# Performance work log

Hardware: AMD Instinct MI355X
Metric: run time of the kernel (lower is better)

The kernel has to match this reference:

```python
import jax, jax.numpy as jnp
import numpy as np

N, DIN, D, K0, NC = 32768, 768, 512, 128, 2
KS = [128, 64, 32, 16]  # prototype counts per stage (num_protos // 2**i)
NEG_SLOPE = 0.01


def _lin(x, W, b):
    # torch nn.Linear: W is [out, in]
    return x @ W.T + b


def _ln(x, g, b):
    m = x.mean(-1, keepdims=True)
    v = ((x - m) ** 2).mean(-1, keepdims=True)
    return (x - m) * jax.lax.rsqrt(v + 1e-5) * g + b


def setup_inputs() -> dict:
    key = jax.random.key(0)
    ks = jax.random.split(key, 40)
    s = 0.02

    def nrm(k, shp, sc=s):
        return jax.random.normal(k, shp, jnp.float32) * sc

    inp = {}
    inp["data"] = jax.random.normal(ks[0], (N, DIN), jnp.float32)
    inp["prototypes"] = jax.random.normal(ks[1], (K0, DIN), jnp.float32)
    inp["W_pp"] = nrm(ks[2], (D, DIN)); inp["b_pp"] = jnp.zeros((D,), jnp.float32)
    inp["W_cp"] = nrm(ks[3], (D, DIN)); inp["b_cp"] = jnp.zeros((D,), jnp.float32)
    inp["sim_scale"] = jnp.ones((1,), jnp.float32)
    # 3 enhancer MLPs + layernorms (stacked, same shapes)
    inp["enh_w1"] = nrm(ks[4], (3, D, D)); inp["enh_b1"] = jnp.zeros((3, D), jnp.float32)
    inp["enh_w2"] = nrm(ks[5], (3, D, D)); inp["enh_b2"] = jnp.zeros((3, D), jnp.float32)
    inp["ln_g"] = jnp.ones((3, D), jnp.float32); inp["ln_b"] = jnp.zeros((3, D), jnp.float32)
    # ProtoReducers: Mlp along K axis; fc1 [inK,inK], fc2 [outK,inK]
    ki = 6
    for i in range(3):
        inK, outK = KS[i], KS[i + 1]
        inp[f"red_w1_{i}"] = nrm(ks[ki], (inK, inK)); ki += 1
        inp[f"red_b1_{i}"] = jnp.zeros((inK,), jnp.float32)
        inp[f"red_w2_{i}"] = nrm(ks[ki], (outK, inK)); ki += 1
        inp[f"red_b2_{i}"] = jnp.zeros((outK,), jnp.float32)
    inp["W_proc"] = nrm(ks[20], (D, D)); inp["b_proc"] = jnp.zeros((D,), jnp.float32)
    inp["g_an"] = jnp.ones((D,), jnp.float32); inp["b_an"] = jnp.zeros((D,), jnp.float32)
    inp["W_t"] = nrm(ks[21], (D, D)); inp["b_t"] = jnp.zeros((D,), jnp.float32)
    inp["W_g"] = nrm(ks[22], (D, D)); inp["b_g"] = jnp.zeros((D,), jnp.float32)
    inp["W_s"] = nrm(ks[23], (1, D)); inp["b_s"] = jnp.zeros((1,), jnp.float32)
    inp["W_h"] = nrm(ks[24], (D, D)); inp["b_h"] = jnp.zeros((D,), jnp.float32)
    inp["W_c"] = nrm(ks[25], (NC, D)); inp["b_c"] = jnp.zeros((NC,), jnp.float32)
    return inp


def reference(data, prototypes, W_pp, b_pp, W_cp, b_cp, sim_scale,
              enh_w1, enh_b1, enh_w2, enh_b2, ln_g, ln_b,
              red_w1_0, red_b1_0, red_w2_0, red_b2_0,
              red_w1_1, red_b1_1, red_w2_1, red_b2_1,
              red_w1_2, red_b1_2, red_w2_2, red_b2_2,
              W_proc, b_proc, g_an, b_an,
              W_t, b_t, W_g, b_g, W_s, b_s, W_h, b_h, W_c, b_c):
    # patch / prototype projections (Linear + LeakyReLU)
    P = jax.nn.leaky_relu(_lin(data, W_pp, b_pp), NEG_SLOPE)        # [N, D]
    C = jax.nn.leaky_relu(_lin(prototypes, W_cp, b_cp), NEG_SLOPE)  # [K0, D]
    # denom = max(1e-6, tau * similarity_scale.item()); tau=1, no grad through scale
    denom = jnp.maximum(1e-6, jax.lax.stop_gradient(sim_scale)[0])
    reds = [(red_w1_0, red_b1_0, red_w2_0, red_b2_0),
            (red_w1_1, red_b1_1, red_w2_1, red_b2_1),
            (red_w1_2, red_b1_2, red_w2_2, red_b2_2)]
    for i in range(3):
        # L2 similarity: -cdist(P, C) computed as a GEMM
        d2 = (jnp.sum(P * P, -1, keepdims=True) + jnp.sum(C * C, -1)[None, :]
              - 2.0 * (P @ C.T))
        sim = -jnp.sqrt(jnp.maximum(d2, 1e-12))                     # [N, K]
        A = jax.nn.softmax(sim / denom, axis=1)                     # soft routing
        ctx = A @ C                                                 # [N, D]
        P = _ln(P + ctx, ln_g[i], ln_b[i])
        P = P + _lin(jax.nn.relu(_lin(P, enh_w1[i], enh_b1[i])), enh_w2[i], enh_b2[i])
        # ProtoReducer: Mlp over K axis (operate on C.T of shape [D, K])
        w1, b1, w2, b2 = reds[i]
        Ct = _lin(jax.nn.relu(_lin(C.T, w1, b1)), w2, b2)           # [D, Kout]
        C = Ct.T
    Z = jnp.concatenate([P, C], axis=0)                             # [N+16, D]
    Z = jax.nn.relu(_lin(Z, W_proc, b_proc))
    Z = _ln(Z, g_an, b_an)
    # gated attention MIL pooling
    t = jnp.tanh(_lin(Z, W_t, b_t))
    g = jax.nn.sigmoid(_lin(Z, W_g, b_g))
    scores = _lin(t * g, W_s, b_s)                                  # [N+16, 1]
    Aw = jax.nn.softmax(scores, axis=0)
    bag = Aw.T @ Z                                                  # [1, D]
    h = jax.nn.relu(_lin(bag, W_h, b_h))
    logits = _lin(h, W_c, b_c)                                      # [1, 2]
    return logits
```

## Files before the change

kernel.cpp:

```cpp
#include <hip/hip_runtime.h>
#include <math.h>

typedef _Float16 f16x8 __attribute__((ext_vector_type(8)));
typedef _Float16 f16x4 __attribute__((ext_vector_type(4)));
typedef float f32x4 __attribute__((ext_vector_type(4)));

#define TBM 256
#define TBN 128
#define TBK 32

#define AS1 __attribute__((address_space(1)))
#define AS3 __attribute__((address_space(3)))

__device__ __forceinline__ void gll16(const _Float16* g, _Float16* l)
{
    __builtin_amdgcn_global_load_lds((const AS1 unsigned int*)g,
                                     (AS3 unsigned int*)l, 16, 0, 0);
}

__device__ __forceinline__ int xcd_swz(int d, int nwg)
{
    int q = nwg >> 3, r = nwg & 7;
    int x = d & 7, idx = d >> 3;
    int base = x < r ? x * (q + 1) : r * (q + 1) + (x - r) * q;
    return base + idx;
}

__device__ __forceinline__ float fsigmoid(float x)
{
    return __builtin_amdgcn_rcpf(1.f + __expf(-x));
}
__device__ __forceinline__ float ftanh(float x)
{
    float ax = fabsf(x);
    float e = __expf(-2.f * ax);
    float t = (1.f - e) * __builtin_amdgcn_rcpf(1.f + e);
    return copysignf(t, x);
}

struct CvtSegs {
    const float* src[7];
    _Float16* dst[7];
    int cum4[8];
};

__global__ __launch_bounds__(256)
void cvtall_k(CvtSegs a)
{
    int total = a.cum4[7];
    for (int i = blockIdx.x * 256 + threadIdx.x; i < total; i += gridDim.x * 256) {
        int s = 0;
        while (i >= a.cum4[s + 1]) s++;
        int loc = (i - a.cum4[s]) * 4;
        float4 v = *(const float4*)(a.src[s] + loc);
        f16x4 h = { (_Float16)v.x, (_Float16)v.y, (_Float16)v.z, (_Float16)v.w };
        *(f16x4*)(a.dst[s] + loc) = h;
    }
}

template<int ACT, bool F16OUT>
__global__ __launch_bounds__(256)
void dot_k(const float* __restrict__ X, const float* __restrict__ W,
           const float* __restrict__ bias, void* __restrict__ Yv,
           int M, int K)
{
    int gw = (blockIdx.x * 256 + threadIdx.x) >> 6;
    int lane = threadIdx.x & 63;
    if (gw >= M * 512) return;
    int r = gw >> 9, n = gw & 511;
    const float* xr = X + (size_t)r * K;
    const float* wr = W + (size_t)n * K;
    float d = 0.f;
    for (int t = 0; t < K; t += 256) {
        float4 a = *(const float4*)(xr + t + lane * 4);
        float4 b = *(const float4*)(wr + t + lane * 4);
        d += a.x * b.x + a.y * b.y + a.z * b.z + a.w * b.w;
    }
#pragma unroll
    for (int o = 32; o; o >>= 1) d += __shfl_xor(d, o);
    if (lane == 0) {
        float v = d + bias[n];
        if (ACT == 1) v = v > 0.f ? v : 0.01f * v;
        else if (ACT == 2) v = fmaxf(v, 0.f);
        if (F16OUT) ((_Float16*)Yv)[(size_t)r * 512 + n] = (_Float16)v;
        else        ((float*)Yv)[(size_t)r * 512 + n] = v;
    }
}

__global__ __launch_bounds__(256)
void cvtC2_k(const float* __restrict__ C, _Float16* __restrict__ Ch,
             _Float16* __restrict__ CTh, float* __restrict__ Csq2, int Kin)
{
    int w = threadIdx.x >> 6, lane = threadIdx.x & 63;
    int row = blockIdx.x * 4 + w;
    if (row >= Kin) return;
    float4 a = *(const float4*)(C + (size_t)row * 512 + lane * 8);
    float4 b = *(const float4*)(C + (size_t)row * 512 + lane * 8 + 4);
    f16x8 h;
    h[0] = (_Float16)a.x; h[1] = (_Float16)a.y; h[2] = (_Float16)a.z; h[3] = (_Float16)a.w;
    h[4] = (_Float16)b.x; h[5] = (_Float16)b.y; h[6] = (_Float16)b.z; h[7] = (_Float16)b.w;
    *(f16x8*)(Ch + (size_t)row * 512 + lane * 8) = h;
    float s = 0.f;
#pragma unroll
    for (int q = 0; q < 8; q++) {
        float f = (float)h[q];
        s += f * f;
        CTh[(size_t)(lane * 8 + q) * Kin + row] = h[q];
    }
#pragma unroll
    for (int o = 32; o; o >>= 1) s += __shfl_xor(s, o);
    if (lane == 0) { Csq2[row * 2] = s; Csq2[row * 2 + 1] = 0.f; }
}

template<int MODE, int ACT, bool SQ>
__global__ __launch_bounds__(512)
void mgemm(const _Float16* __restrict__ A, const _Float16* __restrict__ B,
           const float* __restrict__ bias, _Float16* __restrict__ Yh,
           float* __restrict__ Psq4, int M, int K, int Nout)
{
    __shared__ _Float16 As[2][TBM * TBK];
    __shared__ _Float16 Bs[2][TBN * TBK];
    const int tid = threadIdx.x;
    const int lane = tid & 63;
    const int wid = tid >> 6;
    const int wr = wid >> 1, wc = wid & 1;

    int bid = xcd_swz(blockIdx.y * gridDim.x + blockIdx.x, gridDim.x * gridDim.y);
    const int m0 = (bid / gridDim.x) * TBM;
    const int n0 = (bid % gridDim.x) * TBN;

    f32x4 acc[4][4] = {};
    const int nt = K / TBK;

    const int lrow = lane >> 2;
    const int lk = (lane & 3) * 8;

    auto stage = [&](int t, int buf) {
        const int k0 = t * TBK;
#pragma unroll
        for (int q = 0; q < 2; q++) {
            int c = wid * 2 + q;
            int r = c * 16 + lrow;
            int am = min(m0 + r, M - 1);
            gll16(A + (size_t)am * K + k0 + lk, &As[buf][c * 512]);
        }
        {
            int c = wid;
            int r = c * 16 + lrow;
            int bn = min(n0 + r, Nout - 1);
            gll16(B + (size_t)bn * K + k0 + lk, &Bs[buf][c * 512]);
        }
    };

    stage(0, 0);
    __syncthreads();
    for (int t = 0; t < nt; ++t) {
        const int cur = t & 1;
        if (t + 1 < nt) stage(t + 1, cur ^ 1);
        f16x8 af[4], bf[4];
#pragma unroll
        for (int mi = 0; mi < 4; mi++)
            af[mi] = *(const f16x8*)(&As[cur][(wr * 64 + mi * 16 + (lane & 15)) * TBK + (lane >> 4) * 8]);
#pragma unroll
        for (int nj = 0; nj < 4; nj++)
            bf[nj] = *(const f16x8*)(&Bs[cur][(wc * 64 + nj * 16 + (lane & 15)) * TBK + (lane >> 4) * 8]);
#pragma unroll
        for (int mi = 0; mi < 4; mi++)
#pragma unroll
            for (int nj = 0; nj < 4; nj++)
                acc[mi][nj] = __builtin_amdgcn_mfma_f32_16x16x32_f16(af[mi], bf[nj], acc[mi][nj], 0, 0, 0);
        __syncthreads();
    }

    _Float16* eb = &As[0][0];
    const int g = lane >> 4;
#pragma unroll
    for (int p = 0; p < 2; p++) {
        if (p) __syncthreads();
        if ((wr >> 1) == p) {
#pragma unroll
            for (int nj = 0; nj < 4; nj++) {
                int col = wc * 64 + nj * 16 + (lane & 15);
                float bv = bias ? bias[n0 + col] : 0.f;
#pragma unroll
                for (int mi = 0; mi < 4; mi++)
#pragma unroll
                    for (int r = 0; r < 4; r++) {
                        int lr = (wr & 1) * 64 + mi * 16 + g * 4 + r;
                        float v = acc[mi][nj][r] + bv;
                        if (MODE == 0) {
                            if (ACT == 1) v = v > 0.f ? v : 0.01f * v;
                            else if (ACT == 2) v = fmaxf(v, 0.f);
                        }
                        eb[lr * 128 + col] = (_Float16)v;
                    }
            }
        }
        __syncthreads();
        int t4 = tid * 4;
        int lr = t4 >> 4;
        int cbase = (t4 & 15) * 8;
        int m = m0 + p * 128 + lr;
        float sq = 0.f;
        if (m < M) {
#pragma unroll
            for (int q = 0; q < 4; q++) {
                int c0 = cbase + q * 8;
                f16x8 hv = *(f16x8*)(eb + lr * 128 + c0);
                size_t gidx = (size_t)m * Nout + n0 + c0;
                if (MODE == 1) {
                    f16x8 old = *(f16x8*)(Yh + gidx);
                    f16x8 nw;
#pragma unroll
                    for (int e = 0; e < 8; e++) {
                        float s = (float)old[e] + (float)hv[e];
                        nw[e] = (_Float16)s;
                    }
                    *(f16x8*)(Yh + gidx) = nw;
                    hv = nw;
                } else {
                    *(f16x8*)(Yh + gidx) = hv;
                }
                if (SQ) {
#pragma unroll
                    for (int e = 0; e < 8; e++) { float f = (float)hv[e]; sq += f * f; }
                }
            }
        }
        if (SQ) {
            sq += __shfl_xor(sq, 1);
            sq += __shfl_xor(sq, 2);
            if ((lane & 3) == 0 && m < M) Psq4[(size_t)m * 4 + (n0 >> 7)] = sq;
        }
    }
}

__global__ __launch_bounds__(512)
void ctxln_k(const _Float16* __restrict__ A, const _Float16* __restrict__ CT,
             const float* __restrict__ g, const float* __restrict__ b,
             _Float16* __restrict__ Ph, int M, int Kin)
{
    __shared__ _Float16 As[2][128 * TBK];
    __shared__ _Float16 Bs[2][512 * TBK];
    const int tid = threadIdx.x;
    const int lane = tid & 63;
    const int wid = tid >> 6;
    const int wr = wid >> 2, wc = wid & 3;
    const int m0 = blockIdx.y * 128;

    f32x4 acc[4][8] = {};
    const int nt = Kin / TBK;

    const int lrow = lane >> 2;
    const int lk = (lane & 3) * 8;

    auto stage = [&](int t, int buf) {
        const int k0 = t * TBK;
        {
            int r = wid * 16 + lrow;
            gll16(A + (size_t)(m0 + r) * Kin + k0 + lk, &As[buf][wid * 512]);
        }
#pragma unroll
        for (int q = 0; q < 4; q++) {
            int c = wid * 4 + q;
            int n = c * 16 + lrow;
            gll16(CT + (size_t)n * Kin + k0 + lk, &Bs[buf][c * 512]);
        }
    };

    stage(0, 0);
    __syncthreads();
    for (int t = 0; t < nt; ++t) {
        const int cur = t & 1;
        if (t + 1 < nt) stage(t + 1, cur ^ 1);
        f16x8 af[4], bf[8];
#pragma unroll
        for (int mi = 0; mi < 4; mi++)
            af[mi] = *(const f16x8*)(&As[cur][(wr * 64 + mi * 16 + (lane & 15)) * TBK + (lane >> 4) * 8]);
#pragma unroll
        for (int nj = 0; nj < 8; nj++)
            bf[nj] = *(const f16x8*)(&Bs[cur][(wc * 128 + nj * 16 + (lane & 15)) * TBK + (lane >> 4) * 8]);
#pragma unroll
        for (int mi = 0; mi < 4; mi++)
#pragma unroll
            for (int nj = 0; nj < 8; nj++)
                acc[mi][nj] = __builtin_amdgcn_mfma_f32_16x16x32_f16(af[mi], bf[nj], acc[mi][nj], 0, 0, 0);
        __syncthreads();
    }

    _Float16* eb = &Bs[0][0];
    const int gq = lane >> 4;
#pragma unroll
    for (int p = 0; p < 2; p++) {
        if (p) __syncthreads();
        if (wr == p) {
#pragma unroll
            for (int nj = 0; nj < 8; nj++) {
                int col = wc * 128 + nj * 16 + (lane & 15);
#pragma unroll
                for (int mi = 0; mi < 4; mi++)
#pragma unroll
                    for (int r = 0; r < 4; r++) {
                        int lr = mi * 16 + gq * 4 + r;
                        eb[lr * 512 + col] = (_Float16)acc[mi][nj][r];
                    }
            }
        }
        __syncthreads();
#pragma unroll
        for (int rr = 0; rr < 8; rr++) {
            int lr = wid * 8 + rr;
            int m = m0 + p * 64 + lr;
            f16x8 cv = *(f16x8*)(eb + lr * 512 + lane * 8);
            f16x8 pv = *(const f16x8*)(Ph + (size_t)m * 512 + lane * 8);
            float v[8];
            float s = 0.f, ss = 0.f;
#pragma unroll
            for (int q = 0; q < 8; q++) {
                v[q] = (float)pv[q] + (float)cv[q];
                s += v[q]; ss += v[q] * v[q];
            }
#pragma unroll
            for (int o = 32; o; o >>= 1) { s += __shfl_xor(s, o); ss += __shfl_xor(ss, o); }
            float mean = s * (1.f / 512.f);
            float var = ss * (1.f / 512.f) - mean * mean;
            float inv = 1.f / sqrtf(var + 1e-5f);
            int d0 = lane * 8;
            f16x8 o8;
#pragma unroll
            for (int q = 0; q < 8; q++)
                o8[q] = (_Float16)((v[q] - mean) * inv * g[d0 + q] + b[d0 + q]);
            *(f16x8*)(Ph + (size_t)m * 512 + d0) = o8;
        }
    }
}

__global__ __launch_bounds__(512)
void procln_k(const _Float16* __restrict__ A, const _Float16* __restrict__ W,
              const float* __restrict__ bias, const float* __restrict__ g,
              const float* __restrict__ b, _Float16* __restrict__ Zh, int M)
{
    __shared__ _Float16 As[2][128 * TBK];
    __shared__ _Float16 Bs[2][512 * TBK];
    const int tid = threadIdx.x;
    const int lane = tid & 63;
    const int wid = tid >> 6;
    const int wr = wid >> 2, wc = wid & 3;
    const int m0 = blockIdx.y * 128;
    const int K = 512;

    f32x4 acc[4][8] = {};
    const int nt = K / TBK;

    const int lrow = lane >> 2;
    const int lk = (lane & 3) * 8;

    auto stage = [&](int t, int buf) {
        const int k0 = t * TBK;
        {
            int r = wid * 16 + lrow;
            gll16(A + (size_t)(m0 + r) * K + k0 + lk, &As[buf][wid * 512]);
        }
#pragma unroll
        for (int q = 0; q < 4; q++) {
            int c = wid * 4 + q;
            int n = c * 16 + lrow;
            gll16(W + (size_t)n * K + k0 + lk, &Bs[buf][c * 512]);
        }
    };

    stage(0, 0);
    __syncthreads();
    for (int t = 0; t < nt; ++t) {
        const int cur = t & 1;
        if (t + 1 < nt) stage(t + 1, cur ^ 1);
        f16x8 af[4], bf[8];
#pragma unroll
        for (int mi = 0; mi < 4; mi++)
            af[mi] = *(const f16x8*)(&As[cur][(wr * 64 + mi * 16 + (lane & 15)) * TBK + (lane >> 4) * 8]);
#pragma unroll
        for (int nj = 0; nj < 8; nj++)
            bf[nj] = *(const f16x8*)(&Bs[cur][(wc * 128 + nj * 16 + (lane & 15)) * TBK + (lane >> 4) * 8]);
#pragma unroll
        for (int mi = 0; mi < 4; mi++)
#pragma unroll
            for (int nj = 0; nj < 8; nj++)
                acc[mi][nj] = __builtin_amdgcn_mfma_f32_16x16x32_f16(af[mi], bf[nj], acc[mi][nj], 0, 0, 0);
        __syncthreads();
    }

    _Float16* eb = &Bs[0][0];
    const int gq = lane >> 4;
#pragma unroll
    for (int p = 0; p < 2; p++) {
        if (p) __syncthreads();
        if (wr == p) {
#pragma unroll
            for (int nj = 0; nj < 8; nj++) {
                int col = wc * 128 + nj * 16 + (lane & 15);
                float bv = bias[col];
#pragma unroll
                for (int mi = 0; mi < 4; mi++)
#pragma unroll
                    for (int r = 0; r < 4; r++) {
                        int lr = mi * 16 + gq * 4 + r;
                        eb[lr * 512 + col] = (_Float16)fmaxf(acc[mi][nj][r] + bv, 0.f);
                    }
            }
        }
        __syncthreads();
#pragma unroll
        for (int rr = 0; rr < 8; rr++) {
            int lr = wid * 8 + rr;
            int m = m0 + p * 64 + lr;
            f16x8 cv = *(f16x8*)(eb + lr * 512 + lane * 8);
            float v[8];
            float s = 0.f, ss = 0.f;
#pragma unroll
            for (int q = 0; q < 8; q++) {
                v[q] = (float)cv[q];
                s += v[q]; ss += v[q] * v[q];
            }
#pragma unroll
            for (int o = 32; o; o >>= 1) { s += __shfl_xor(s, o); ss += __shfl_xor(ss, o); }
            float mean = s * (1.f / 512.f);
            float var = ss * (1.f / 512.f) - mean * mean;
            float inv = 1.f / sqrtf(var + 1e-5f);
            int d0 = lane * 8;
            f16x8 o8;
#pragma unroll
            for (int q = 0; q < 8; q++)
                o8[q] = (_Float16)((v[q] - mean) * inv * g[d0 + q] + b[d0 + q]);
            *(f16x8*)(Zh + (size_t)m * 512 + d0) = o8;
        }
    }
}

__global__ __launch_bounds__(512)
void gatgemm(const _Float16* __restrict__ A, const _Float16* __restrict__ B1,
             const _Float16* __restrict__ B2, const float* __restrict__ c1,
             const float* __restrict__ c2, const float* __restrict__ Ws,
             float* __restrict__ scr4, int M, int K, int Nout)
{
    __shared__ _Float16 As[2][TBM * TBK];
    __shared__ _Float16 B1s[2][TBN * TBK];
    __shared__ _Float16 B2s[2][TBN * TBK];
    const int tid = threadIdx.x;
    const int lane = tid & 63;
    const int wid = tid >> 6;
    const int wr = wid >> 1, wc = wid & 1;

    int bid = xcd_swz(blockIdx.y * gridDim.x + blockIdx.x, gridDim.x * gridDim.y);
    const int m0 = (bid / gridDim.x) * TBM;
    const int n0 = (bid % gridDim.x) * TBN;

    f32x4 acc1[4][4] = {};
    f32x4 acc2[4][4] = {};
    const int nt = K / TBK;

    const int lrow = lane >> 2;
    const int lk = (lane & 3) * 8;

    auto stage = [&](int t, int buf) {
        const int k0 = t * TBK;
#pragma unroll
        for (int q = 0; q < 2; q++) {
            int c = wid * 2 + q;
            int r = c * 16 + lrow;
            int am = min(m0 + r, M - 1);
            gll16(A + (size_t)am * K + k0 + lk, &As[buf][c * 512]);
        }
        {
            int c = wid;
            int r = c * 16 + lrow;
            int bn = min(n0 + r, Nout - 1);
            gll16(B1 + (size_t)bn * K + k0 + lk, &B1s[buf][c * 512]);
            gll16(B2 + (size_t)bn * K + k0 + lk, &B2s[buf][c * 512]);
        }
    };

    stage(0, 0);
    __syncthreads();
    for (int t = 0; t < nt; ++t) {
        const int cur = t & 1;
        if (t + 1 < nt) stage(t + 1, cur ^ 1);
        f16x8 af[4], bf1[4], bf2[4];
#pragma unroll
        for (int mi = 0; mi < 4; mi++)
            af[mi] = *(const f16x8*)(&As[cur][(wr * 64 + mi * 16 + (lane & 15)) * TBK + (lane >> 4) * 8]);
#pragma unroll
        for (int nj = 0; nj < 4; nj++) {
            int ro = (wc * 64 + nj * 16 + (lane & 15)) * TBK + (lane >> 4) * 8;
            bf1[nj] = *(const f16x8*)(&B1s[cur][ro]);
            bf2[nj] = *(const f16x8*)(&B2s[cur][ro]);
        }
#pragma unroll
        for (int mi = 0; mi < 4; mi++)
#pragma unroll
            for (int nj = 0; nj < 4; nj++) {
                acc1[mi][nj] = __builtin_amdgcn_mfma_f32_16x16x32_f16(af[mi], bf1[nj], acc1[mi][nj], 0, 0, 0);
                acc2[mi][nj] = __builtin_amdgcn_mfma_f32_16x16x32_f16(af[mi], bf2[nj], acc2[mi][nj], 0, 0, 0);
            }
        __syncthreads();
    }

    const int g = lane >> 4;
    float wsv[4];
#pragma unroll
    for (int nj = 0; nj < 4; nj++)
        wsv[nj] = Ws[n0 + wc * 64 + nj * 16 + (lane & 15)];
#pragma unroll
    for (int mi = 0; mi < 4; mi++) {
#pragma unroll
        for (int r = 0; r < 4; r++) {
            float p = 0.f;
#pragma unroll
            for (int nj = 0; nj < 4; nj++) {
                int col = n0 + wc * 64 + nj * 16 + (lane & 15);
                float t1 = ftanh(acc1[mi][nj][r] + c1[col]);
                float g1 = fsigmoid(acc2[mi][nj][r] + c2[col]);
                p += t1 * g1 * wsv[nj];
            }
#pragma unroll
            for (int o = 1; o < 16; o <<= 1) p += __shfl_xor(p, o);
            if ((lane & 15) == 0) {
                int m = m0 + wr * 64 + mi * 16 + g * 4 + r;
                if (m < M) scr4[(size_t)m * 4 + (n0 >> 7)] = p;
            }
        }
    }
}

#define SBM 128
__global__ __launch_bounds__(256)
void simgemm(const _Float16* __restrict__ A, const _Float16* __restrict__ B,
             const float* __restrict__ Psq4, const float* __restrict__ Csq2,
             const float* __restrict__ sscale, _Float16* __restrict__ Ah,
             int M, int K)
{
    const int Kin = 128;
    __shared__ _Float16 As[2][SBM * TBK];
    __shared__ _Float16 Bs[2][SBM * TBK];
    __shared__ float redmx[2][SBM];
    __shared__ float redsm[2][SBM];
    const int tid = threadIdx.x;
    const int lane = tid & 63;
    const int wid = tid >> 6;
    const int wr = wid >> 1, wc = wid & 1;
    const int m0 = blockIdx.y * SBM;

    f32x4 acc[4][4] = {};
    const int nt = K / TBK;
    const int lrow = lane >> 2;
    const int lk = (lane & 3) * 8;

    auto stage = [&](int t, int buf) {
        const int k0 = t * TBK;
#pragma unroll
        for (int q = 0; q < 2; q++) {
            int c = wid * 2 + q;
            int r = c * 16 + lrow;
            gll16(A + (size_t)(m0 + r) * K + k0 + lk, &As[buf][c * 512]);
            gll16(B + (size_t)r * K + k0 + lk, &Bs[buf][c * 512]);
        }
    };

    stage(0, 0);
    __syncthreads();
    for (int t = 0; t < nt; ++t) {
        const int cur = t & 1;
        if (t + 1 < nt) stage(t + 1, cur ^ 1);
        f16x8 af[4], bf[4];
#pragma unroll
        for (int mi = 0; mi < 4; mi++)
            af[mi] = *(const f16x8*)(&As[cur][(wr * 64 + mi * 16 + (lane & 15)) * TBK + (lane >> 4) * 8]);
#pragma unroll
        for (int nj = 0; nj < 4; nj++)
            bf[nj] = *(const f16x8*)(&Bs[cur][(wc * 64 + nj * 16 + (lane & 15)) * TBK + (lane >> 4) * 8]);
#pragma unroll
        for (int mi = 0; mi < 4; mi++)
#pragma unroll
            for (int nj = 0; nj < 4; nj++)
                acc[mi][nj] = __builtin_amdgcn_mfma_f32_16x16x32_f16(af[mi], bf[nj], acc[mi][nj], 0, 0, 0);
        __syncthreads();
    }

// ... 225 lines not shown
}

__global__ __launch_bounds__(1024)
void pool_k(const float4* __restrict__ s4, float* __restrict__ s,
            float* __restrict__ scal, int M)
{
    __shared__ float sm[16];
    int tid = threadIdx.x, lane = tid & 63, wid = tid >> 6;
    float mx = -INFINITY;
    for (int i = tid; i < M; i += 1024) {
        float4 a = s4[i];
        float v = (a.x + a.y) + (a.z + a.w);
        s[i] = v;
        mx = fmaxf(mx, v);
    }
#pragma unroll
    for (int o = 32; o; o >>= 1) mx = fmaxf(mx, __shfl_xor(mx, o));
    if (lane == 0) sm[wid] = mx;
    __syncthreads();
    if (wid == 0) {
        float v = (lane < 16) ? sm[lane] : -INFINITY;
#pragma unroll
        for (int o = 8; o; o >>= 1) v = fmaxf(v, __shfl_xor(v, o));
        if (lane == 0) sm[0] = v;
    }
    __syncthreads();
    float gmax = sm[0];
    __syncthreads();
    float sum = 0.f;
    for (int i = tid; i < M; i += 1024) {
        float e = __expf(s[i] - gmax);
        s[i] = e;
        sum += e;
    }
#pragma unroll
    for (int o = 32; o; o >>= 1) sum += __shfl_xor(sum, o);
    if (lane == 0) sm[wid] = sum;
    __syncthreads();
    if (tid == 0) {
        float t = 0.f;
        for (int w = 0; w < 16; w++) t += sm[w];
        scal[0] = t;
    }
}

__global__ __launch_bounds__(256)
void bagp_k(const _Float16* __restrict__ Z, const float* __restrict__ w,
            float* __restrict__ PB, int M, int cs)
{
    int d = blockIdx.x * 256 + threadIdx.x;
    int chunk = blockIdx.y;
    int i0 = chunk * cs;
    int i1 = min(M, i0 + cs);
    float acc = 0.f;
    for (int i = i0; i < i1; i++) acc = fmaf(w[i], (float)Z[(size_t)i * 512 + d], acc);
    PB[(size_t)chunk * 512 + d] = acc;
}

__global__ __launch_bounds__(256)
void bagf_k(const float* __restrict__ PB, const float* __restrict__ scal,
            float* __restrict__ bag, int nchunk)
{
    int d = blockIdx.x * 256 + threadIdx.x;
    float acc = 0.f;
    for (int c = 0; c < nchunk; c++) acc += PB[(size_t)c * 512 + d];
    bag[d] = acc / scal[0];
}

__global__ __launch_bounds__(256)
void h_k(const float* __restrict__ bag, const float* __restrict__ Wh,
         const float* __restrict__ bh, float* __restrict__ h)
{
    int wid = threadIdx.x >> 6, lane = threadIdx.x & 63;
    int j = blockIdx.x * 4 + wid;
    const float* wr = Wh + (size_t)j * 512;
    float d = 0.f;
#pragma unroll
    for (int t = 0; t < 2; t++) {
        float4 a = *(const float4*)(wr + t * 256 + lane * 4);
        float4 bv = *(const float4*)(bag + t * 256 + lane * 4);
        d += a.x * bv.x + a.y * bv.y + a.z * bv.z + a.w * bv.w;
    }
#pragma unroll
    for (int o = 32; o; o >>= 1) d += __shfl_xor(d, o);
    if (lane == 0) h[j] = fmaxf(d + bh[j], 0.f);
}

__global__ __launch_bounds__(128)
void logit_k(const float* __restrict__ h, const float* __restrict__ Wc,
             const float* __restrict__ bc, float* __restrict__ out)
{
    int wid = threadIdx.x >> 6, lane = threadIdx.x & 63;
    const float* wr = Wc + (size_t)wid * 512;
    float d = 0.f;
#pragma unroll
    for (int t = 0; t < 2; t++) {
        float4 a = *(const float4*)(wr + t * 256 + lane * 4);
        float4 hv = *(const float4*)(h + t * 256 + lane * 4);
        d += a.x * hv.x + a.y * hv.y + a.z * hv.z + a.w * hv.w;
    }
#pragma unroll
    for (int o = 32; o; o >>= 1) d += __shfl_xor(d, o);
    if (lane == 0) out[wid] = d + bc[wid];
}

extern "C" void kernel_launch(void* const* d_in, const int* in_sizes, int n_in,
                              void* d_out, int out_size, void* d_ws, size_t ws_size,
                              hipStream_t stream)
{
    const float* data    = (const float*)d_in[0];
    const float* protos  = (const float*)d_in[1];
    const float* W_pp    = (const float*)d_in[2];
    const float* b_pp    = (const float*)d_in[3];
    const float* W_cp    = (const float*)d_in[4];
    const float* b_cp    = (const float*)d_in[5];
    const float* sscale  = (const float*)d_in[6];
    const float* enh_w1  = (const float*)d_in[7];
    const float* enh_b1  = (const float*)d_in[8];
    const float* enh_w2  = (const float*)d_in[9];
    const float* enh_b2  = (const float*)d_in[10];
    const float* ln_g    = (const float*)d_in[11];
    const float* ln_b    = (const float*)d_in[12];
    const float* red_w1[3] = {(const float*)d_in[13], (const float*)d_in[17], (const float*)d_in[21]};
    const float* red_b1[3] = {(const float*)d_in[14], (const float*)d_in[18], (const float*)d_in[22]};
    const float* red_w2[3] = {(const float*)d_in[15], (const float*)d_in[19], (const float*)d_in[23]};
    const float* red_b2[3] = {(const float*)d_in[16], (const float*)d_in[20], (const float*)d_in[24]};
    const float* W_proc  = (const float*)d_in[25];
    const float* b_proc  = (const float*)d_in[26];
    const float* g_an    = (const float*)d_in[27];
    const float* b_an    = (const float*)d_in[28];
    const float* W_t     = (const float*)d_in[29];
    const float* b_t     = (const float*)d_in[30];
    const float* W_g     = (const float*)d_in[31];
    const float* b_g     = (const float*)d_in[32];
    const float* W_s     = (const float*)d_in[33];
    const float* b_s     = (const float*)d_in[34];
    const float* W_h     = (const float*)d_in[35];
    const float* b_h     = (const float*)d_in[36];
    const float* W_c     = (const float*)d_in[37];
    const float* b_c     = (const float*)d_in[38];
    float* out = (float*)d_out;
    (void)b_s;

    constexpr int N = 32768, DIN = 768, D = 512;
    constexpr int NCHUNK = 256;
    char* w = (char*)d_ws;
    auto alloc = [&](size_t bytes) -> char* {
        char* p = w; w += (bytes + 255) & ~(size_t)255; return p;
    };
    _Float16* Ph     = (_Float16*)alloc((size_t)N * D * 2);
    _Float16* TMPh   = (_Float16*)alloc((size_t)N * D * 2);
    _Float16* Zh     = (_Float16*)alloc((size_t)(N + 16) * D * 2);
    _Float16* Ztail  = (_Float16*)alloc((size_t)16 * D * 2);
    _Float16* datah  = (_Float16*)alloc((size_t)N * DIN * 2);
    _Float16* Ah     = (_Float16*)alloc((size_t)N * 128 * 2);
    _Float16* Ch     = (_Float16*)alloc(128 * D * 2);
    _Float16* CTh    = (_Float16*)alloc(128 * D * 2);
    _Float16* Wpph   = (_Float16*)alloc((size_t)D * DIN * 2);
    _Float16* w1h    = (_Float16*)alloc((size_t)3 * D * D * 2);
    _Float16* w2h    = (_Float16*)alloc((size_t)3 * D * D * 2);
    _Float16* Wproch = (_Float16*)alloc((size_t)D * D * 2);
    _Float16* Wth    = (_Float16*)alloc((size_t)D * D * 2);
    _Float16* Wgh    = (_Float16*)alloc((size_t)D * D * 2);
    float*    Psq4   = (float*)alloc((size_t)N * 4 * 4);
    float*    Csq2   = (float*)alloc(128 * 2 * 4);
    float*    Ca     = (float*)alloc(128 * D * 4);
    float*    Cb     = (float*)alloc(128 * D * 4);
    float*    H1     = (float*)alloc(128 * D * 4);
    float*    scr4   = (float*)alloc((size_t)(N + 16) * 4 * 4);
    float*    scr    = (float*)alloc((size_t)(N + 16) * 4);
    float*    PB     = (float*)alloc((size_t)NCHUNK * D * 4);
    float*    bag    = (float*)alloc(D * 4);
    float*    hb     = (float*)alloc(D * 4);
    float*    scal   = (float*)alloc(8 * 4);

    dim3 blk(256);
    dim3 blk512(512);
    auto mgrid = [](int M_, int Nout_) { return dim3((Nout_ + TBN - 1) / TBN, (M_ + TBM - 1) / TBM); };

    {
        CvtSegs cs;
        const float* srcs[7] = { data, W_pp, enh_w1, enh_w2, W_proc, W_t, W_g };
        _Float16* dsts[7]    = { datah, Wpph, w1h, w2h, Wproch, Wth, Wgh };
        int sizes[7] = { N * DIN, D * DIN, 3 * D * D, 3 * D * D, D * D, D * D, D * D };
        int c = 0;
        cs.cum4[0] = 0;
        for (int s = 0; s < 7; s++) {
            cs.src[s] = srcs[s]; cs.dst[s] = dsts[s];
            c += sizes[s] / 4;
            cs.cum4[s + 1] = c;
        }
        cvtall_k<<<dim3(4096), blk, 0, stream>>>(cs);
    }

    mgemm<0, 1, true><<<mgrid(N, D), blk512, 0, stream>>>(datah, Wpph, b_pp, Ph, Psq4, N, DIN, D);
    dot_k<1, false><<<dim3(128 * 512 / 4), blk, 0, stream>>>(protos, W_cp, b_cp, Ca, 128, DIN);
    cvtC2_k<<<dim3(32), blk, 0, stream>>>(Ca, Ch, CTh, Csq2, 128);

    float* C = Ca;
    float* Cn = Cb;
    int Kin = 128;
    for (int i = 0; i < 3; i++) {
        int Kout = Kin >> 1;
        if (i == 0)
            simgemm<<<dim3(1, N / SBM), blk, 0, stream>>>(Ph, Ch, Psq4, Csq2, sscale, Ah, N, D);
        else if (i == 1)
            simgemm_s<64><<<dim3(1, N / 256), blk, 0, stream>>>(Ph, Ch, Psq4, Csq2, sscale, Ah, N, D);
        else
            simgemm_s<32><<<dim3(1, N / 256), blk, 0, stream>>>(Ph, Ch, Psq4, Csq2, sscale, Ah, N, D);
        ctxln_k<<<dim3(1, N / 128), blk512, 0, stream>>>(Ah, CTh, ln_g + (size_t)i * D, ln_b + (size_t)i * D, Ph, N, Kin);
        mgemm<0, 2, false><<<mgrid(N, D), blk512, 0, stream>>>(Ph, w1h + (size_t)i * D * D, enh_b1 + (size_t)i * D, TMPh, nullptr, N, D, D);
        if (i < 2)
            mgemm<1, 0, true><<<mgrid(N, D), blk512, 0, stream>>>(TMPh, w2h + (size_t)i * D * D, enh_b2 + (size_t)i * D, Ph, Psq4, N, D, D);
        else
            mgemm<1, 0, false><<<mgrid(N, D), blk512, 0, stream>>>(TMPh, w2h + (size_t)i * D * D, enh_b2 + (size_t)i * D, Ph, nullptr, N, D, D);
        red1_k<<<dim3(2, Kin), blk, 0, stream>>>(C, red_w1[i], red_b1[i], H1, Kin);
        red2_k<<<dim3(2, Kout), blk, 0, stream>>>(H1, red_w2[i], red_b2[i], Cn, Ch, CTh, Csq2, Kin, Kout);
        float* t = C; C = Cn; Cn = t;
        Kin = Kout;
    }

    procln_k<<<dim3(1, N / 128), blk512, 0, stream>>>(Ph, Wproch, b_proc, g_an, b_an, Zh, N);
    dot_k<2, true><<<dim3(16 * 512 / 4), blk, 0, stream>>>(C, W_proc, b_proc, Ztail, 16, D);
    ln_k<<<dim3(4), blk, 0, stream>>>(Ztail, nullptr, g_an, b_an, Zh + (size_t)N * D, 16);

    gatgemm<<<mgrid(N + 16, D), blk512, 0, stream>>>(Zh, Wth, Wgh, b_t, b_g, W_s, scr4, N + 16, D, D);

    pool_k<<<dim3(1), dim3(1024), 0, stream>>>((const float4*)scr4, scr, scal, N + 16);
    int cs2 = (N + 16 + NCHUNK - 1) / NCHUNK;
    bagp_k<<<dim3(2, NCHUNK), blk, 0, stream>>>(Zh, scr, PB, N + 16, cs2);
    bagf_k<<<dim3(2), blk, 0, stream>>>(PB, scal, bag, NCHUNK);

    h_k<<<dim3(128), blk, 0, stream>>>(bag, W_h, b_h, hb);
    logit_k<<<dim3(1), dim3(128), 0, stream>>>(hb, W_c, b_c, out);
}
```

Before: 772.5 us.

## Fuse fp32-to-fp16 conversion of input data into the first projection GEMM

The separate pass that converted the 32768x768 fp32 data matrix to fp16 is removed, and a new GEMM kernel reads fp32 data directly, converts in registers and writes fp16 into LDS. This drops one full write and re-read of the fp16 copy of the data. In exchange the A-tile loads become synchronous register loads instead of direct global-to-LDS loads, which reduces overlap inside the GEMM and doubles the bytes read for A. The conversion kernel's grid is also halved since it now only handles weights.

```diff
diff --git a/kernel.cpp b/kernel.cpp
--- a/kernel.cpp
+++ b/kernel.cpp
@@ -39,15 +39,15 @@
 }
 
 struct CvtSegs {
-    const float* src[7];
-    _Float16* dst[7];
-    int cum4[8];
+    const float* src[6];
+    _Float16* dst[6];
+    int cum4[7];
 };
 
 __global__ __launch_bounds__(256)
 void cvtall_k(CvtSegs a)
 {
-    int total = a.cum4[7];
+    int total = a.cum4[6];
     for (int i = blockIdx.x * 256 + threadIdx.x; i < total; i += gridDim.x * 256) {
         int s = 0;
         while (i >= a.cum4[s + 1]) s++;
@@ -232,6 +232,114 @@
             sq += __shfl_xor(sq, 2);
             if ((lane & 3) == 0 && m < M) Psq4[(size_t)m * 4 + (n0 >> 7)] = sq;
         }
+    }
+}
+
+__global__ __launch_bounds__(512)
+void pgemm32(const float* __restrict__ A32, const _Float16* __restrict__ B,
+             const float* __restrict__ bias, _Float16* __restrict__ Yh,
+             float* __restrict__ Psq4, int M, int K, int Nout)
+{
+    __shared__ _Float16 As[2][TBM * TBK];
+    __shared__ _Float16 Bs[2][TBN * TBK];
+    const int tid = threadIdx.x;
+    const int lane = tid & 63;
+    const int wid = tid >> 6;
+    const int wr = wid >> 1, wc = wid & 1;
+
+    int bid = xcd_swz(blockIdx.y * gridDim.x + blockIdx.x, gridDim.x * gridDim.y);
+    const int m0 = (bid / gridDim.x) * TBM;
+    const int n0 = (bid % gridDim.x) * TBN;
+
+    f32x4 acc[4][4] = {};
+    const int nt = K / TBK;
+
+    const int lrow = lane >> 2;
+    const int lk = (lane & 3) * 8;
+
+    auto stage = [&](int t, int buf) {
+        const int k0 = t * TBK;
+#pragma unroll
+        for (int q = 0; q < 2; q++) {
+            int c = wid * 2 + q;
+            int r = c * 16 + lrow;
+            int am = min(m0 + r, M - 1);
+            const float* src = A32 + (size_t)am * K + k0 + lk;
+            float4 a0 = *(const float4*)src;
+            float4 a1 = *(const float4*)(src + 4);
+            f16x8 h;
+            h[0] = (_Float16)a0.x; h[1] = (_Float16)a0.y; h[2] = (_Float16)a0.z; h[3] = (_Float16)a0.w;
+            h[4] = (_Float16)a1.x; h[5] = (_Float16)a1.y; h[6] = (_Float16)a1.z; h[7] = (_Float16)a1.w;
+            *(f16x8*)(&As[buf][c * 512 + lane * 8]) = h;
+        }
+        {
+            int c = wid;
+            int r = c * 16 + lrow;
+            int bn = min(n0 + r, Nout - 1);
+            gll16(B + (size_t)bn * K + k0 + lk, &Bs[buf][c * 512]);
+        }
+    };
+
+    stage(0, 0);
+    __syncthreads();
+    for (int t = 0; t < nt; ++t) {
+        const int cur = t & 1;
+        if (t + 1 < nt) stage(t + 1, cur ^ 1);
+        f16x8 af[4], bf[4];
+#pragma unroll
+        for (int mi = 0; mi < 4; mi++)
+            af[mi] = *(const f16x8*)(&As[cur][(wr * 64 + mi * 16 + (lane & 15)) * TBK + (lane >> 4) * 8]);
+#pragma unroll
+        for (int nj = 0; nj < 4; nj++)
+            bf[nj] = *(const f16x8*)(&Bs[cur][(wc * 64 + nj * 16 + (lane & 15)) * TBK + (lane >> 4) * 8]);
+#pragma unroll
+        for (int mi = 0; mi < 4; mi++)
+#pragma unroll
+            for (int nj = 0; nj < 4; nj++)
+                acc[mi][nj] = __builtin_amdgcn_mfma_f32_16x16x32_f16(af[mi], bf[nj], acc[mi][nj], 0, 0, 0);
+        __syncthreads();
+    }
+
+    _Float16* eb = &As[0][0];
+    const int g = lane >> 4;
+#pragma unroll
+    for (int p = 0; p < 2; p++) {
+        if (p) __syncthreads();
+        if ((wr >> 1) == p) {
+#pragma unroll
+            for (int nj = 0; nj < 4; nj++) {
+                int col = wc * 64 + nj * 16 + (lane & 15);
+                float bv = bias[n0 + col];
+#pragma unroll
+                for (int mi = 0; mi < 4; mi++)
+#pragma unroll
+                    for (int r = 0; r < 4; r++) {
+                        int lr = (wr & 1) * 64 + mi * 16 + g * 4 + r;
+                        float v = acc[mi][nj][r] + bv;
+                        v = v > 0.f ? v : 0.01f * v;
+                        eb[lr * 128 + col] = (_Float16)v;
+                    }
+            }
+        }
+        __syncthreads();
+        int t4 = tid * 4;
+        int lr = t4 >> 4;
+        int cbase = (t4 & 15) * 8;
+        int m = m0 + p * 128 + lr;
+        float sq = 0.f;
+        if (m < M) {
+#pragma unroll
+            for (int q = 0; q < 4; q++) {
+                int c0 = cbase + q * 8;
+                f16x8 hv = *(f16x8*)(eb + lr * 128 + c0);
+                *(f16x8*)(Yh + (size_t)m * Nout + n0 + c0) = hv;
+#pragma unroll
+                for (int e = 0; e < 8; e++) { float f = (float)hv[e]; sq += f * f; }
+            }
+        }
+        sq += __shfl_xor(sq, 1);
+        sq += __shfl_xor(sq, 2);
+        if ((lane & 3) == 0 && m < M) Psq4[(size_t)m * 4 + (n0 >> 7)] = sq;
     }
 }
 
@@ -963,7 +1071,6 @@
     _Float16* TMPh   = (_Float16*)alloc((size_t)N * D * 2);
     _Float16* Zh     = (_Float16*)alloc((size_t)(N + 16) * D * 2);
     _Float16* Ztail  = (_Float16*)alloc((size_t)16 * D * 2);
-    _Float16* datah  = (_Float16*)alloc((size_t)N * DIN * 2);
     _Float16* Ah     = (_Float16*)alloc((size_t)N * 128 * 2);
     _Float16* Ch     = (_Float16*)alloc(128 * D * 2);
     _Float16* CTh    = (_Float16*)alloc(128 * D * 2);
@@ -991,20 +1098,20 @@
 
     {
         CvtSegs cs;
-        const float* srcs[7] = { data, W_pp, enh_w1, enh_w2, W_proc, W_t, W_g };
-        _Float16* dsts[7]    = { datah, Wpph, w1h, w2h, Wproch, Wth, Wgh };
-        int sizes[7] = { N * DIN, D * DIN, 3 * D * D, 3 * D * D, D * D, D * D, D * D };
+        const float* srcs[6] = { W_pp, enh_w1, enh_w2, W_proc, W_t, W_g };
+        _Float16* dsts[6]    = { Wpph, w1h, w2h, Wproch, Wth, Wgh };
+        int sizes[6] = { D * DIN, 3 * D * D, 3 * D * D, D * D, D * D, D * D };
         int c = 0;
         cs.cum4[0] = 0;
-        for (int s = 0; s < 7; s++) {
+        for (int s = 0; s < 6; s++) {
             cs.src[s] = srcs[s]; cs.dst[s] = dsts[s];
             c += sizes[s] / 4;
             cs.cum4[s + 1] = c;
         }
-        cvtall_k<<<dim3(4096), blk, 0, stream>>>(cs);
-    }
-
-    mgemm<0, 1, true><<<mgrid(N, D), blk512, 0, stream>>>(datah, Wpph, b_pp, Ph, Psq4, N, DIN, D);
+        cvtall_k<<<dim3(2048), blk, 0, stream>>>(cs);
+    }
+
+    pgemm32<<<mgrid(N, D), blk512, 0, stream>>>(data, Wpph, b_pp, Ph, Psq4, N, DIN, D);
     dot_k<1, false><<<dim3(128 * 512 / 4), blk, 0, stream>>>(protos, W_cp, b_cp, Ca, 128, DIN);
     cvtC2_k<<<dim3(32), blk, 0, stream>>>(Ca, Ch, CTh, Csq2, 128);
 
```

New measurement: 757.7 us. No clear change (-1.9%).

## Fuse fp32 input conversion into projection GEMM; add triple-buffered full-row MLP GEMM

Applied to the files above, without the earlier changes.

The separate fp32-to-fp16 conversion of the large data matrix is removed. The first projection GEMM now loads fp32 rows directly and converts them to fp16 while staging into LDS, which avoids writing a half-precision copy and reading it back. The enhancer MLP GEMMs and the processing GEMM+LayerNorm now share one 128x512-tile kernel. It uses a three-stage async global-to-LDS pipeline with fine-grained barriers, interleaved prefetch and s_setprio around the MFMA bursts. The cost is that the fp32 A loads in the first GEMM are synchronous register loads rather than async LDS loads, so their latency may be less hidden.

```diff
diff --git a/kernel.cpp b/kernel.cpp
--- a/kernel.cpp
+++ b/kernel.cpp
@@ -39,15 +39,15 @@
 }
 
 struct CvtSegs {
-    const float* src[7];
-    _Float16* dst[7];
-    int cum4[8];
+    const float* src[6];
+    _Float16* dst[6];
+    int cum4[7];
 };
 
 __global__ __launch_bounds__(256)
 void cvtall_k(CvtSegs a)
 {
-    int total = a.cum4[7];
+    int total = a.cum4[6];
     for (int i = blockIdx.x * 256 + threadIdx.x; i < total; i += gridDim.x * 256) {
         int s = 0;
         while (i >= a.cum4[s + 1]) s++;
@@ -112,11 +112,10 @@
     if (lane == 0) { Csq2[row * 2] = s; Csq2[row * 2 + 1] = 0.f; }
 }
 
-template<int MODE, int ACT, bool SQ>
 __global__ __launch_bounds__(512)
-void mgemm(const _Float16* __restrict__ A, const _Float16* __restrict__ B,
-           const float* __restrict__ bias, _Float16* __restrict__ Yh,
-           float* __restrict__ Psq4, int M, int K, int Nout)
+void pgemm32(const float* __restrict__ A32, const _Float16* __restrict__ B,
+             const float* __restrict__ bias, _Float16* __restrict__ Yh,
+             float* __restrict__ Psq4, int M, int K, int Nout)
 {
     __shared__ _Float16 As[2][TBM * TBK];
     __shared__ _Float16 Bs[2][TBN * TBK];
@@ -142,7 +141,13 @@
             int c = wid * 2 + q;
             int r = c * 16 + lrow;
             int am = min(m0 + r, M - 1);
-            gll16(A + (size_t)am * K + k0 + lk, &As[buf][c * 512]);
+            const float* src = A32 + (size_t)am * K + k0 + lk;
+            float4 a0 = *(const float4*)src;
+            float4 a1 = *(const float4*)(src + 4);
+            f16x8 h;
+            h[0] = (_Float16)a0.x; h[1] = (_Float16)a0.y; h[2] = (_Float16)a0.z; h[3] = (_Float16)a0.w;
+            h[4] = (_Float16)a1.x; h[5] = (_Float16)a1.y; h[6] = (_Float16)a1.z; h[7] = (_Float16)a1.w;
+            *(f16x8*)(&As[buf][c * 512 + lane * 8]) = h;
         }
         {
             int c = wid;
@@ -181,17 +186,14 @@
 #pragma unroll
             for (int nj = 0; nj < 4; nj++) {
                 int col = wc * 64 + nj * 16 + (lane & 15);
-                float bv = bias ? bias[n0 + col] : 0.f;
+                float bv = bias[n0 + col];
 #pragma unroll
                 for (int mi = 0; mi < 4; mi++)
 #pragma unroll
                     for (int r = 0; r < 4; r++) {
                         int lr = (wr & 1) * 64 + mi * 16 + g * 4 + r;
                         float v = acc[mi][nj][r] + bv;
-                        if (MODE == 0) {
-                            if (ACT == 1) v = v > 0.f ? v : 0.01f * v;
-                            else if (ACT == 2) v = fmaxf(v, 0.f);
-                        }
+                        v = v > 0.f ? v : 0.01f * v;
                         eb[lr * 128 + col] = (_Float16)v;
                     }
             }
@@ -207,30 +209,157 @@
             for (int q = 0; q < 4; q++) {
                 int c0 = cbase + q * 8;
                 f16x8 hv = *(f16x8*)(eb + lr * 128 + c0);
-                size_t gidx = (size_t)m * Nout + n0 + c0;
-                if (MODE == 1) {
-                    f16x8 old = *(f16x8*)(Yh + gidx);
-                    f16x8 nw;
-#pragma unroll
-                    for (int e = 0; e < 8; e++) {
-                        float s = (float)old[e] + (float)hv[e];
-                        nw[e] = (_Float16)s;
+                *(f16x8*)(Yh + (size_t)m * Nout + n0 + c0) = hv;
+#pragma unroll
+                for (int e = 0; e < 8; e++) { float f = (float)hv[e]; sq += f * f; }
+            }
+        }
+        sq += __shfl_xor(sq, 1);
+        sq += __shfl_xor(sq, 2);
+        if ((lane & 3) == 0 && m < M) Psq4[(size_t)m * 4 + (n0 >> 7)] = sq;
+    }
+}
+
+template<int EPI, bool SQ>
+__global__ __launch_bounds__(512)
+void mlp8p_k(const _Float16* __restrict__ A, const _Float16* __restrict__ W,
+             const float* __restrict__ bias, const float* __restrict__ g,
+             const float* __restrict__ b, _Float16* __restrict__ Y,
+             float* __restrict__ Psq4, int M)
+{
+    __shared__ _Float16 As[3][128 * 32];
+    __shared__ _Float16 Bs[3][512 * 32];
+    const int tid = threadIdx.x;
+    const int lane = tid & 63;
+    const int wid = tid >> 6;
+    const int wr = wid >> 2, wc = wid & 3;
+    const int m0 = blockIdx.y * 128;
+    const int K = 512;
+    const int nt = 16;
+
+    f32x4 acc[4][8] = {};
+    const int lrow = lane >> 2;
+    const int lk = (lane & 3) * 8;
+
+    auto stageA = [&](int t, int buf) {
+        int r = wid * 16 + lrow;
+        gll16(A + (size_t)(m0 + r) * K + t * 32 + lk, &As[buf][wid * 512]);
+    };
+    auto stageB = [&](int t, int buf, int q) {
+        int c = wid * 4 + q;
+        int n = c * 16 + lrow;
+        gll16(W + (size_t)n * K + t * 32 + lk, &Bs[buf][c * 512]);
+    };
+
+    stageA(0, 0);
+#pragma unroll
+    for (int q = 0; q < 4; q++) stageB(0, 0, q);
+    stageA(1, 1);
+#pragma unroll
+    for (int q = 0; q < 4; q++) stageB(1, 1, q);
+
+    for (int t = 0; t < nt; ++t) {
+        const int cur = t % 3;
+        const int nbuf = (t + 2) % 3;
+        const bool pf = (t + 2) < nt;
+        if (t + 1 < nt) asm volatile("s_waitcnt vmcnt(5)" ::: "memory");
+        else            asm volatile("s_waitcnt vmcnt(0)" ::: "memory");
+        __builtin_amdgcn_s_barrier();
+
+        f16x8 af[4];
+#pragma unroll
+        for (int p = 0; p < 4; p++) {
+            if (p == 0) {
+#pragma unroll
+                for (int mi = 0; mi < 4; mi++)
+                    af[mi] = *(const f16x8*)(&As[cur][(wr * 64 + mi * 16 + (lane & 15)) * 32 + (lane >> 4) * 8]);
+            }
+            f16x8 bf0 = *(const f16x8*)(&Bs[cur][(wc * 128 + (2 * p) * 16 + (lane & 15)) * 32 + (lane >> 4) * 8]);
+            f16x8 bf1 = *(const f16x8*)(&Bs[cur][(wc * 128 + (2 * p + 1) * 16 + (lane & 15)) * 32 + (lane >> 4) * 8]);
+            if (pf) {
+                if (p == 0) { stageA(t + 2, nbuf); stageB(t + 2, nbuf, 0); }
+                else stageB(t + 2, nbuf, p);
+            }
+            __builtin_amdgcn_s_barrier();
+            __builtin_amdgcn_s_setprio(1);
+#pragma unroll
+            for (int mi = 0; mi < 4; mi++) {
+                acc[mi][2 * p]     = __builtin_amdgcn_mfma_f32_16x16x32_f16(af[mi], bf0, acc[mi][2 * p], 0, 0, 0);
+                acc[mi][2 * p + 1] = __builtin_amdgcn_mfma_f32_16x16x32_f16(af[mi], bf1, acc[mi][2 * p + 1], 0, 0, 0);
+            }
+            __builtin_amdgcn_s_setprio(0);
+            __builtin_amdgcn_s_barrier();
+        }
+    }
+
+    _Float16* eb = &Bs[0][0];
+    const int gq = lane >> 4;
+#pragma unroll
+    for (int p = 0; p < 2; p++) {
+        if (p) __syncthreads();
+        if (wr == p) {
+#pragma unroll
+            for (int nj = 0; nj < 8; nj++) {
+                int col = wc * 128 + nj * 16 + (lane & 15);
+                float bv = bias[col];
+#pragma unroll
+                for (int mi = 0; mi < 4; mi++)
+#pragma unroll
+                    for (int r = 0; r < 4; r++) {
+                        int lr = mi * 16 + gq * 4 + r;
+                        float v = acc[mi][nj][r] + bv;
+                        if (EPI == 0 || EPI == 2) v = fmaxf(v, 0.f);
+                        eb[lr * 512 + col] = (_Float16)v;
                     }
-                    *(f16x8*)(Yh + gidx) = nw;
-                    hv = nw;
-                } else {
-                    *(f16x8*)(Yh + gidx) = hv;
+            }
+        }
+        __syncthreads();
+#pragma unroll
+        for (int rr = 0; rr < 8; rr++) {
+            int lr = wid * 8 + rr;
+            int m = m0 + p * 64 + lr;
+            f16x8 cv = *(f16x8*)(eb + lr * 512 + lane * 8);
+            if (EPI == 0) {
+                *(f16x8*)(Y + (size_t)m * 512 + lane * 8) = cv;
+            } else if (EPI == 1) {
+                f16x8 pv = *(const f16x8*)(Y + (size_t)m * 512 + lane * 8);
+                f16x8 o8;
+                float sq = 0.f;
+#pragma unroll
+                for (int q = 0; q < 8; q++) {
+                    float s = (float)pv[q] + (float)cv[q];
+                    o8[q] = (_Float16)s;
+                    if (SQ) { float f = (float)o8[q]; sq += f * f; }
                 }
+                *(f16x8*)(Y + (size_t)m * 512 + lane * 8) = o8;
                 if (SQ) {
 #pragma unroll
-                    for (int e = 0; e < 8; e++) { float f = (float)hv[e]; sq += f * f; }
+                    for (int o = 32; o; o >>= 1) sq += __shfl_xor(sq, o);
+                    if (lane == 0) {
+                        float4 w4 = { sq, 0.f, 0.f, 0.f };
+                        *(float4*)(Psq4 + (size_t)m * 4) = w4;
+                    }
                 }
-            }
-        }
-        if (SQ) {
-            sq += __shfl_xor(sq, 1);
-            sq += __shfl_xor(sq, 2);
-            if ((lane & 3) == 0 && m < M) Psq4[(size_t)m * 4 + (n0 >> 7)] = sq;
+            } else {
+                float v[8];
+                float s = 0.f, ss = 0.f;
+#pragma unroll
+                for (int q = 0; q < 8; q++) {
+                    v[q] = (float)cv[q];
+                    s += v[q]; ss += v[q] * v[q];
+                }
+#pragma unroll
+                for (int o = 32; o; o >>= 1) { s += __shfl_xor(s, o); ss += __shfl_xor(ss, o); }
+                float mean = s * (1.f / 512.f);
+                float var = ss * (1.f / 512.f) - mean * mean;
+                float inv = 1.f / sqrtf(var + 1e-5f);
+                int d0 = lane * 8;
+                f16x8 o8;
+#pragma unroll
+                for (int q = 0; q < 8; q++)
+                    o8[q] = (_Float16)((v[q] - mean) * inv * g[d0 + q] + b[d0 + q]);
+                *(f16x8*)(Y + (size_t)m * 512 + d0) = o8;
+            }
         }
     }
 }
@@ -250,7 +379,6 @@
 
     f32x4 acc[4][8] = {};
     const int nt = Kin / TBK;
-
     const int lrow = lane >> 2;
     const int lk = (lane & 3) * 8;
 
@@ -331,107 +459,6 @@
             for (int q = 0; q < 8; q++)
                 o8[q] = (_Float16)((v[q] - mean) * inv * g[d0 + q] + b[d0 + q]);
             *(f16x8*)(Ph + (size_t)m * 512 + d0) = o8;
-        }
-    }
-}
-
-__global__ __launch_bounds__(512)
-void procln_k(const _Float16* __restrict__ A, const _Float16* __restrict__ W,
-              const float* __restrict__ bias, const float* __restrict__ g,
-              const float* __restrict__ b, _Float16* __restrict__ Zh, int M)
-{
-    __shared__ _Float16 As[2][128 * TBK];
-    __shared__ _Float16 Bs[2][512 * TBK];
-    const int tid = threadIdx.x;
-    const int lane = tid & 63;
-    const int wid = tid >> 6;
-    const int wr = wid >> 2, wc = wid & 3;
-    const int m0 = blockIdx.y * 128;
-    const int K = 512;
-
-    f32x4 acc[4][8] = {};
-    const int nt = K / TBK;
-
-    const int lrow = lane >> 2;
-    const int lk = (lane & 3) * 8;
-
-    auto stage = [&](int t, int buf) {
-        const int k0 = t * TBK;
-        {
-            int r = wid * 16 + lrow;
-            gll16(A + (size_t)(m0 + r) * K + k0 + lk, &As[buf][wid * 512]);
-        }
-#pragma unroll
-        for (int q = 0; q < 4; q++) {
-            int c = wid * 4 + q;
-            int n = c * 16 + lrow;
-            gll16(W + (size_t)n * K + k0 + lk, &Bs[buf][c * 512]);
-        }
-    };
-
-    stage(0, 0);
-    __syncthreads();
-    for (int t = 0; t < nt; ++t) {
-        const int cur = t & 1;
-        if (t + 1 < nt) stage(t + 1, cur ^ 1);
-        f16x8 af[4], bf[8];
-#pragma unroll
-        for (int mi = 0; mi < 4; mi++)
-            af[mi] = *(const f16x8*)(&As[cur][(wr * 64 + mi * 16 + (lane & 15)) * TBK + (lane >> 4) * 8]);
-#pragma unroll
-        for (int nj = 0; nj < 8; nj++)
-            bf[nj] = *(const f16x8*)(&Bs[cur][(wc * 128 + nj * 16 + (lane & 15)) * TBK + (lane >> 4) * 8]);
-#pragma unroll
-        for (int mi = 0; mi < 4; mi++)
-#pragma unroll
-            for (int nj = 0; nj < 8; nj++)
-                acc[mi][nj] = __builtin_amdgcn_mfma_f32_16x16x32_f16(af[mi], bf[nj], acc[mi][nj], 0, 0, 0);
-        __syncthreads();
-    }
-
-    _Float16* eb = &Bs[0][0];
-    const int gq = lane >> 4;
-#pragma unroll
-    for (int p = 0; p < 2; p++) {
-        if (p) __syncthreads();
-        if (wr == p) {
-#pragma unroll
-            for (int nj = 0; nj < 8; nj++) {
-                int col = wc * 128 + nj * 16 + (lane & 15);
-                float bv = bias[col];
-#pragma unroll
-                for (int mi = 0; mi < 4; mi++)
-#pragma unroll
-                    for (int r = 0; r < 4; r++) {
-                        int lr = mi * 16 + gq * 4 + r;
-                        eb[lr * 512 + col] = (_Float16)fmaxf(acc[mi][nj][r] + bv, 0.f);
-                    }
-            }
-        }
-        __syncthreads();
-#pragma unroll
-        for (int rr = 0; rr < 8; rr++) {
-            int lr = wid * 8 + rr;
-            int m = m0 + p * 64 + lr;
-            f16x8 cv = *(f16x8*)(eb + lr * 512 + lane * 8);
-            float v[8];
-            float s = 0.f, ss = 0.f;
-#pragma unroll
-            for (int q = 0; q < 8; q++) {
-                v[q] = (float)cv[q];
-                s += v[q]; ss += v[q] * v[q];
-            }
-#pragma unroll
-            for (int o = 32; o; o >>= 1) { s += __shfl_xor(s, o); ss += __shfl_xor(ss, o); }
-            float mean = s * (1.f / 512.f);
-            float var = ss * (1.f / 512.f) - mean * mean;
-            float inv = 1.f / sqrtf(var + 1e-5f);
-            int d0 = lane * 8;
-            f16x8 o8;
-#pragma unroll
-            for (int q = 0; q < 8; q++)
-                o8[q] = (_Float16)((v[q] - mean) * inv * g[d0 + q] + b[d0 + q]);
-            *(f16x8*)(Zh + (size_t)m * 512 + d0) = o8;
         }
     }
 }
@@ -963,7 +990,6 @@
     _Float16* TMPh   = (_Float16*)alloc((size_t)N * D * 2);
     _Float16* Zh     = (_Float16*)alloc((size_t)(N + 16) * D * 2);
     _Float16* Ztail  = (_Float16*)alloc((size_t)16 * D * 2);
-    _Float16* datah  = (_Float16*)alloc((size_t)N * DIN * 2);
     _Float16* Ah     = (_Float16*)alloc((size_t)N * 128 * 2);
     _Float16* Ch     = (_Float16*)alloc(128 * D * 2);
     _Float16* CTh    = (_Float16*)alloc(128 * D * 2);
@@ -991,20 +1017,20 @@
 
     {
         CvtSegs cs;
-        const float* srcs[7] = { data, W_pp, enh_w1, enh_w2, W_proc, W_t, W_g };
-        _Float16* dsts[7]    = { datah, Wpph, w1h, w2h, Wproch, Wth, Wgh };
-        int sizes[7] = { N * DIN, D * DIN, 3 * D * D, 3 * D * D, D * D, D * D, D * D };
+        const float* srcs[6] = { W_pp, enh_w1, enh_w2, W_proc, W_t, W_g };
+        _Float16* dsts[6]    = { Wpph, w1h, w2h, Wproch, Wth, Wgh };
+        int sizes[6] = { D * DIN, 3 * D * D, 3 * D * D, D * D, D * D, D * D };
         int c = 0;
         cs.cum4[0] = 0;
-        for (int s = 0; s < 7; s++) {
+        for (int s = 0; s < 6; s++) {
             cs.src[s] = srcs[s]; cs.dst[s] = dsts[s];
             c += sizes[s] / 4;
             cs.cum4[s + 1] = c;
         }
-        cvtall_k<<<dim3(4096), blk, 0, stream>>>(cs);
-    }
-
-    mgemm<0, 1, true><<<mgrid(N, D), blk512, 0, stream>>>(datah, Wpph, b_pp, Ph, Psq4, N, DIN, D);
+        cvtall_k<<<dim3(2048), blk, 0, stream>>>(cs);
+    }
+
+    pgemm32<<<mgrid(N, D), blk512, 0, stream>>>(data, Wpph, b_pp, Ph, Psq4, N, DIN, D);
     dot_k<1, false><<<dim3(128 * 512 / 4), blk, 0, stream>>>(protos, W_cp, b_cp, Ca, 128, DIN);
     cvtC2_k<<<dim3(32), blk, 0, stream>>>(Ca, Ch, CTh, Csq2, 128);
 
@@ -1020,18 +1046,18 @@
         else
             simgemm_s<32><<<dim3(1, N / 256), blk, 0, stream>>>(Ph, Ch, Psq4, Csq2, sscale, Ah, N, D);
         ctxln_k<<<dim3(1, N / 128), blk512, 0, stream>>>(Ah, CTh, ln_g + (size_t)i * D, ln_b + (size_t)i * D, Ph, N, Kin);
-        mgemm<0, 2, false><<<mgrid(N, D), blk512, 0, stream>>>(Ph, w1h + (size_t)i * D * D, enh_b1 + (size_t)i * D, TMPh, nullptr, N, D, D);
+        mlp8p_k<0, false><<<dim3(1, N / 128), blk512, 0, stream>>>(Ph, w1h + (size_t)i * D * D, enh_b1 + (size_t)i * D, nullptr, nullptr, TMPh, nullptr, N);
         if (i < 2)
-            mgemm<1, 0, true><<<mgrid(N, D), blk512, 0, stream>>>(TMPh, w2h + (size_t)i * D * D, enh_b2 + (size_t)i * D, Ph, Psq4, N, D, D);
+            mlp8p_k<1, true><<<dim3(1, N / 128), blk512, 0, stream>>>(TMPh, w2h + (size_t)i * D * D, enh_b2 + (size_t)i * D, nullptr, nullptr, Ph, Psq4, N);
         else
-            mgemm<1, 0, false><<<mgrid(N, D), blk512, 0, stream>>>(TMPh, w2h + (size_t)i * D * D, enh_b2 + (size_t)i * D, Ph, nullptr, N, D, D);
+            mlp8p_k<1, false><<<dim3(1, N / 128), blk512, 0, stream>>>(TMPh, w2h + (size_t)i * D * D, enh_b2 + (size_t)i * D, nullptr, nullptr, Ph, nullptr, N);
         red1_k<<<dim3(2, Kin), blk, 0, stream>>>(C, red_w1[i], red_b1[i], H1, Kin);
         red2_k<<<dim3(2, Kout), blk, 0, stream>>>(H1, red_w2[i], red_b2[i], Cn, Ch, CTh, Csq2, Kin, Kout);
         float* t = C; C = Cn; Cn = t;
         Kin = Kout;
     }
 
-    procln_k<<<dim3(1, N / 128), blk512, 0, stream>>>(Ph, Wproch, b_proc, g_an, b_an, Zh, N);
+    mlp8p_k<2, false><<<dim3(1, N / 128), blk512, 0, stream>>>(Ph, Wproch, b_proc, g_an, b_an, Zh, nullptr, N);
     dot_k<2, true><<<dim3(16 * 512 / 4), blk, 0, stream>>>(C, W_proc, b_proc, Ztail, 16, D);
     ln_k<<<dim3(4), blk, 0, stream>>>(Ztail, nullptr, g_an, b_an, Zh + (size_t)N * D, 16);
 
```

New measurement: 769.2 us. No clear change (-0.4%).
